# Kernel tuning notes

Measured on AMD Instinct MI355X. Metric: run time of the kernel, lower is better.

The kernel has to match this reference:

```python
import jax, jax.numpy as jnp
import numpy as np

L = 2          # stacked LSTM layers
E = 4          # ensemble size
B, T, D = 256, 256, 512
H, CTX, HID, OUT = 512, 256, 256, 64


def setup_inputs() -> dict:
    key = jax.random.key(0)
    ks = jax.random.split(key, 16)
    w = lambda k, s, sc: (jax.random.normal(k, s, jnp.float32) * sc)
    r1 = lambda k, s: 1.0 + 0.05 * jax.random.normal(k, s, jnp.float32)
    lstm_b = jnp.zeros((L, E, 4 * H), jnp.float32).at[:, :, H:2 * H].set(1.0)  # unit forget bias
    return {
        'sequence_embeddings': jax.random.normal(ks[0], (B, T, D), jnp.float32),
        'context_embeddings': jax.random.normal(ks[1], (B, CTX), jnp.float32),
        'sequence_length': jax.random.randint(ks[2], (B,), 1, T + 1, jnp.int32),
        'lstm_W': w(ks[3], (L, D, 4 * H), 0.02),
        'lstm_U': w(ks[4], (L, H, 4 * H), 0.02),
        'lstm_b': lstm_b,
        'lstm_alpha': r1(ks[5], (L, E, D)),
        'lstm_gamma': r1(ks[6], (L, E, 4 * H)),
        'lstm_ralpha': r1(ks[7], (L, E, H)),
        'lstm_rgamma': r1(ks[8], (L, E, 4 * H)),
        'hid_W': w(ks[9], (H + CTX, HID), 0.05),
        'hid_b': jnp.zeros((E, HID), jnp.float32),
        'hid_alpha': r1(ks[10], (E, H + CTX)),
        'hid_gamma': r1(ks[11], (E, HID)),
        'out_W': w(ks[12], (HID, OUT), 0.05),
        'out_b': jnp.zeros((E, OUT), jnp.float32),
        'out_alpha': r1(ks[13], (E, HID)),
        'out_gamma': r1(ks[14], (E, OUT)),
    }


def reference(sequence_embeddings, context_embeddings, sequence_length,
              lstm_W, lstm_U, lstm_b, lstm_alpha, lstm_gamma, lstm_ralpha, lstm_rgamma,
              hid_W, hid_b, hid_alpha, hid_gamma,
              out_W, out_b, out_alpha, out_gamma):
    Bv, Tv, _ = sequence_embeddings.shape
    Hv = lstm_U.shape[1]
    per = Bv // E  # examples per ensemble member (consecutive blocks)
    exp = lambda p: jnp.repeat(p, per, axis=1)        # [L,E,d] -> [L,B,d]
    aF, gF = exp(lstm_alpha), exp(lstm_gamma)
    raF, rgF = exp(lstm_ralpha), exp(lstm_rgamma)
    bF = exp(lstm_b)

    dt = sequence_embeddings.dtype
    mask = (jnp.arange(Tv)[None, :] < sequence_length[:, None]).astype(dt)  # [B,T]
    xs = (jnp.swapaxes(sequence_embeddings, 0, 1), mask.T[..., None])       # [T,B,D], [T,B,1]

    def step(carry, xm):
        hs, cs = carry
        x, m = xm
        inp = x
        new_h, new_c = [], []
        for l in range(L):
            h, c = hs[l], cs[l]
            # rank-1 multiplicative perturbations fused with gate matmuls
            z = ((inp * aF[l]) @ lstm_W[l]) * gF[l] \
                + ((h * raF[l]) @ lstm_U[l]) * rgF[l] + bF[l]
            i, f, g, o = jnp.split(z, 4, axis=-1)
            c_n = jax.nn.sigmoid(f) * c + jax.nn.sigmoid(i) * jnp.tanh(g)
            h_n = jax.nn.sigmoid(o) * jnp.tanh(c_n)
            h_n = jnp.where(m > 0, h_n, h)  # masked steps carry state through
            c_n = jnp.where(m > 0, c_n, c)
            new_h.append(h_n)
            new_c.append(c_n)
            inp = h_n
        return (jnp.stack(new_h), jnp.stack(new_c)), None

    init = (jnp.zeros((L, Bv, Hv), dt), jnp.zeros((L, Bv, Hv), dt))
    (hs, _), _ = jax.lax.scan(step, init, xs)
    feat = jnp.concatenate([hs[-1], context_embeddings], axis=-1)

    def dense_r1(x, Wt, bt, al, ga, act=None):
        af = jnp.repeat(al, per, axis=0)
        gf = jnp.repeat(ga, per, axis=0)
        bf = jnp.repeat(bt, per, axis=0)
        y = ((x * af) @ Wt) * gf + bf
        return act(y) if act is not None else y

    relu6 = lambda v: jnp.clip(v, 0.0, 6.0)
    hidden = dense_r1(feat, hid_W, hid_b, hid_alpha, hid_gamma, relu6)
    return dense_r1(hidden, out_W, out_b, out_alpha, out_gamma)
```

## Files before the change

### kernel.cpp

```cpp
#include <hip/hip_runtime.h>
#include <cstdint>
#include <cstddef>


typedef __attribute__((ext_vector_type(8))) short  s16x8;
typedef __attribute__((ext_vector_type(8))) __bf16 bf16x8;
typedef __attribute__((ext_vector_type(4))) float  f32x4;
typedef unsigned long long ull;

__device__ __forceinline__ short f2bfs(float f) {
  union { float f; unsigned u; } v; v.f = f;
  unsigned r = v.u + 0x7FFFu + ((v.u >> 16) & 1u);
  return (short)(r >> 16);
}
__device__ __forceinline__ float bf2f(short s) {
  union { unsigned u; float f; } v; v.u = ((unsigned)(unsigned short)s) << 16;
  return v.f;
}
__device__ __forceinline__ void split2(float v, short& hi, short& lo) {
  hi = f2bfs(v);
  lo = f2bfs(v - bf2f(hi));
}
__device__ __forceinline__ float sigf(float x) { return 1.0f / (1.0f + __expf(-x)); }
__device__ __forceinline__ float tanhf_fast(float x) {
  float xc = fminf(fmaxf(x, -15.f), 15.f);
  float e = __expf(2.f * xc);
  return __fdividef(e - 1.f, e + 1.f);
}

__device__ __forceinline__ void unpack_pk(const uint4 r0, const uint4 r1,
                                          s16x8& hi, s16x8& lo) {
  uint4 hv, lv;
  hv.x = __builtin_amdgcn_perm(r0.y, r0.x, 0x05040100u);
  lv.x = __builtin_amdgcn_perm(r0.y, r0.x, 0x07060302u);
  hv.y = __builtin_amdgcn_perm(r0.w, r0.z, 0x05040100u);
  lv.y = __builtin_amdgcn_perm(r0.w, r0.z, 0x07060302u);
  hv.z = __builtin_amdgcn_perm(r1.y, r1.x, 0x05040100u);
  lv.z = __builtin_amdgcn_perm(r1.y, r1.x, 0x07060302u);
  hv.w = __builtin_amdgcn_perm(r1.w, r1.z, 0x05040100u);
  lv.w = __builtin_amdgcn_perm(r1.w, r1.z, 0x07060302u);
  hi = __builtin_bit_cast(s16x8, hv);
  lo = __builtin_bit_cast(s16x8, lv);
}

#define HIP_RLX __ATOMIC_RELAXED
#define HIP_AGT __HIP_MEMORY_SCOPE_AGENT

__device__ __forceinline__ void step_sync(unsigned* grpBase, unsigned* Pme,
                                          unsigned* Pother, int cb,
                                          unsigned tstep, int pneed) {
  __syncthreads();
  if (threadIdx.x < 64) {
    const int lane = threadIdx.x;
    int rel = 0;
    if (lane == 0) {
      unsigned a = __hip_atomic_fetch_add(grpBase + ((cb >> 3) << 4), 1u,
                                          HIP_RLX, HIP_AGT);
      if (a == 8u * tstep - 1u) {
        unsigned r = __hip_atomic_fetch_add(grpBase + 64, 1u, HIP_RLX, HIP_AGT);
        if (r == 4u * tstep - 1u) rel = 1;
      }
    }
    rel = __shfl(rel, 0);
    unsigned* flags = grpBase + 128;
    if (rel) {
      if (lane < 32)
        __hip_atomic_store(flags + lane * 16, tstep, HIP_RLX, HIP_AGT);
      if (lane == 0)
        __hip_atomic_store(Pme, tstep, HIP_RLX, HIP_AGT);
    }
    if (lane == 0) {
      if (!rel) {
        int spins = 0;
        while (__hip_atomic_load(flags + cb * 16, HIP_RLX, HIP_AGT) < tstep) {
          __builtin_amdgcn_s_sleep(1);
          if (++spins > (1 << 24)) break;
        }
      }
      if (pneed > 0) {
        int spins = 0;
        while ((int)__hip_atomic_load(Pother, HIP_RLX, HIP_AGT) < pneed) {
          __builtin_amdgcn_s_sleep(1);
          if (++spins > (1 << 24)) break;
        }
      }
      __builtin_amdgcn_fence(__ATOMIC_ACQUIRE, "agent");
    }
  }
  __syncthreads();
}

#define REDOFF 131072
#define BHU 131072

__global__ __launch_bounds__(512, 1) void lstm_persist(
    const unsigned* __restrict__ seqP,
    unsigned* __restrict__ h0P, unsigned* __restrict__ h1P,
    const short* __restrict__ Wf, const float* __restrict__ biasF,
    const int* __restrict__ slen, unsigned* __restrict__ bar)
{
  extern __shared__ __align__(16) char bsw[];
  const int wg = blockIdx.x;
  const int cls = wg & 7;
  const int layer = cls >> 2;
  const int rb = cls & 3;
  const int cb = wg >> 3;
  const int tid = threadIdx.x;
  const int wave = tid >> 6, lane = tid & 63;
  const int kh = wave >> 2, ws = wave & 3;

  const short* Wfe = Wf + ((size_t)(layer * 4 + rb) * 2048 + cb * 64) * 1024;
  #pragma unroll
  for (int i = 0; i < 16; ++i) {
    int f = (i << 9) + tid;
    int col = f >> 7, fr = f & 127;
    s16x8 v = *reinterpret_cast<const s16x8*>(Wfe + (size_t)col * 1024 + (fr << 3));
    int byo = (fr << 10) + (((col << 4)) ^ ((fr & 7) << 4));
    *reinterpret_cast<s16x8*>(bsw + byo) = v;
  }
  __syncthreads();

  const int j = lane & 15;
  const int g = lane >> 4;
  const int koff = g << 3;
  const int rowg = rb * 64 + ws * 16 + j;
  const int rbase = rb * 64 + ws * 16 + (g << 2);
  const int u = cb * 16 + j;
  const float* bp = biasF + (size_t)(layer * 4 + rb) * 2048 + cb * 64 + j;
  const float bi = bp[0], bff = bp[16], bg = bp[32], bo = bp[48];
  int msl[4];
  #pragma unroll
  for (int r = 0; r < 4; ++r) msl[r] = slen[rbase + r];

  float creg[4] = {0.f, 0.f, 0.f, 0.f};
  float hreg[4] = {0.f, 0.f, 0.f, 0.f};
  unsigned* grpBase = bar + (cls << 10);
  unsigned* Pme     = bar + 8192 + (cls << 4);
  unsigned* Pother  = bar + 8192 + ((cls ^ 4) << 4);
  const int fragbase = kh << 6;

  if (tid == 0) {
    if (layer == 1) {
      int spins = 0;
      while (__hip_atomic_load(Pother, HIP_RLX, HIP_AGT) < 1u) {
        __builtin_amdgcn_s_sleep(1);
        if (++spins > (1 << 24)) break;
      }
    }
    __builtin_amdgcn_fence(__ATOMIC_ACQUIRE, "agent");
  }
  __syncthreads();

  for (int t = 0; t < 256; ++t) {
    const unsigned* ap;
    if (kh == 0) {
      ap = (layer == 0)
         ? seqP + (size_t)t * 131072 + (size_t)rowg * 512 + koff
         : h0P + (size_t)((t + 1) & 3) * BHU + (size_t)rowg * 512 + koff;
    } else {
      ap = (layer == 0)
         ? h0P + (size_t)(t & 3) * BHU + (size_t)rowg * 512 + koff
         : h1P + (size_t)(t & 1) * BHU + (size_t)rowg * 512 + koff;
    }

    uint4 R0[16], R1[16];
    #pragma unroll
    for (int q = 0; q < 16; ++q) {
      R0[q] = *reinterpret_cast<const uint4*>(ap + (q << 5));
      R1[q] = *reinterpret_cast<const uint4*>(ap + (q << 5) + 4);
    }

    f32x4 acc[4] = {}, accL[4] = {};
    #pragma unroll
    for (int q = 0; q < 16; ++q) {
      s16x8 ahi, alo;
      unpack_pk(R0[q], R1[q], ahi, alo);
      const int frag = fragbase + ((q << 2) | g);
      const int fb_ = frag << 10;
      const int xm_ = (frag & 7) << 4;
      #pragma unroll
      for (int cf = 0; cf < 4; ++cf) {
        const int byo_ = fb_ + ((((cf << 8) | (j << 4))) ^ xm_);
        s16x8 b_ = *reinterpret_cast<const s16x8*>(bsw + byo_);
        acc[cf] = __builtin_amdgcn_mfma_f32_16x16x32_bf16(
            __builtin_bit_cast(bf16x8, ahi), __builtin_bit_cast(bf16x8, b_),
            acc[cf], 0, 0, 0);
        accL[cf] = __builtin_amdgcn_mfma_f32_16x16x32_bf16(
            __builtin_bit_cast(bf16x8, alo), __builtin_bit_cast(bf16x8, b_),
            accL[cf], 0, 0, 0);
      }
    }

    if (kh == 1) {
      #pragma unroll
      for (int r = 0; r < 4; ++r) {
        const int lrow = ws * 16 + (g << 2) + r;
        f32x4 v = {acc[0][r] + accL[0][r], acc[1][r] + accL[1][r],
                   acc[2][r] + accL[2][r], acc[3][r] + accL[3][r]};
        *reinterpret_cast<f32x4*>(bsw + REDOFF + lrow * 256 + j * 16) = v;
      }
    }
    __syncthreads();
    if (kh == 0) {
      unsigned* hOut = (layer == 0)
          ? h0P + (size_t)((t + 1) & 3) * BHU
          : h1P + (size_t)((t & 1) ^ 1) * BHU;
      #pragma unroll
      for (int r = 0; r < 4; ++r) {
        const int lrow = ws * 16 + (g << 2) + r;
        f32x4 red = *reinterpret_cast<const f32x4*>(bsw + REDOFF + lrow * 256 + j * 16);
        const int row = rbase + r;
        float zi = acc[0][r] + accL[0][r] + red[0] + bi;
        float zf = acc[1][r] + accL[1][r] + red[1] + bff;
        float zg = acc[2][r] + accL[2][r] + red[2] + bg;
        float zo = acc[3][r] + accL[3][r] + red[3] + bo;
        float cn = sigf(zf) * creg[r] + sigf(zi) * tanhf_fast(zg);
        float hn = sigf(zo) * tanhf_fast(cn);
        if (t >= msl[r]) { cn = creg[r]; hn = hreg[r]; }
        creg[r] = cn; hreg[r] = hn;
        short hh, hl; split2(hn, hh, hl);
        unsigned pk = ((unsigned)(unsigned short)hl << 16)
                    | (unsigned)(unsigned short)hh;
        __hip_atomic_store(&hOut[(size_t)row * 512 + u], pk, HIP_RLX, HIP_AGT);
      }
    }

    int pneed = (t < 255) ? (layer == 0 ? t - 2 : t + 2) : 0;
    step_sync(grpBase, Pme, Pother, cb, (unsigned)(t + 1), pneed);
  }
}

template<int EPI>
__global__ __launch_bounds__(256) void head_gemm(
    const unsigned* __restrict__ a0, int sA0,
    const unsigned* __restrict__ a1, int sA1, int kSplit,
    const short* __restrict__ Wh, const float* __restrict__ bias,
    int N, int K,
    unsigned* __restrict__ outP, float* __restrict__ outf)
{
  const int cb = blockIdx.x, rb = blockIdx.y;
  const int tid = threadIdx.x, wave = tid >> 6, lane = tid & 63;
  const int j = lane & 15;
  const int rowg = rb * 64 + wave * 16 + j;
  const int koff = (lane >> 4) << 3;
  const short* We = Wh + ((size_t)rb * N + cb * 64) * K;
  f32x4 acc[4] = {}, accL[4] = {};
  for (int ks = 0; ks < (K >> 5); ++ks) {
    const int kl = (ks << 5) + koff;
    const unsigned* ap = (kl < kSplit)
        ? (a0 + (size_t)rowg * sA0 + kl)
        : (a1 + (size_t)rowg * sA1 + (kl - kSplit));
    uint4 q0 = *reinterpret_cast<const uint4*>(ap);
    uint4 q1 = *reinterpret_cast<const uint4*>(ap + 4);
    s16x8 ahi, alo; unpack_pk(q0, q1, ahi, alo);
    #pragma unroll
    for (int cf = 0; cf < 4; ++cf) {
      const int ccol = (cf << 4) + j;
      s16x8 b = *reinterpret_cast<const s16x8*>(We + (size_t)ccol * K + kl);
      acc[cf] = __builtin_amdgcn_mfma_f32_16x16x32_bf16(
          __builtin_bit_cast(bf16x8, ahi), __builtin_bit_cast(bf16x8, b),
          acc[cf], 0, 0, 0);
      accL[cf] = __builtin_amdgcn_mfma_f32_16x16x32_bf16(
          __builtin_bit_cast(bf16x8, alo), __builtin_bit_cast(bf16x8, b),
          accL[cf], 0, 0, 0);
    }
  }
  const int rbase = rb * 64 + wave * 16 + ((lane >> 4) << 2);
  #pragma unroll
  for (int cf = 0; cf < 4; ++cf) {
    const int col = cb * 64 + cf * 16 + j;
    const float bb = bias[(size_t)rb * N + col];
    #pragma unroll
    for (int r = 0; r < 4; ++r) {
      float z = acc[cf][r] + accL[cf][r] + bb;
      if (EPI == 1) {
        z = fminf(fmaxf(z, 0.f), 6.f);
        short hh, hl; split2(z, hh, hl);
        outP[(size_t)(rbase + r) * N + col] =
            ((unsigned)(unsigned short)hl << 16) | (unsigned)(unsigned short)hh;
      } else {
        outf[(size_t)(rbase + r) * N + col] = z;
      }
    }
  }
}

__global__ __launch_bounds__(256) void fold_lstm(
    const float* __restrict__ W, const float* __restrict__ U,
    const float* __restrict__ al, const float* __restrict__ ral,
    const float* __restrict__ ga, const float* __restrict__ rga,
    short* __restrict__ Wf)
{
  __shared__ float T[64][65];
  const int tid = threadIdx.x;
  const int kb = blockIdx.x * 64;
  const int cb = blockIdx.y;
  const int le = blockIdx.z;
  const int l  = le >> 2;
  const int kl = tid >> 2;
  const int g  = tid & 3;
  const int k  = kb + kl;
  const bool isW = k < 512;
  const int kk = isW ? k : k - 512;
  const float* src = (isW ? W : U) + ((size_t)l * 512 + kk) * 2048;
  const float  a   = (isW ? al : ral)[(size_t)le * 512 + kk];
  const float* gam = (isW ? ga : rga) + (size_t)le * 2048;
  const int colBase = g * 512 + cb * 16;
  const float4* s4 = reinterpret_cast<const float4*>(src + colBase);
  const float4* g4 = reinterpret_cast<const float4*>(gam + colBase);
  #pragma unroll
  for (int q = 0; q < 4; ++q) {
    float4 v = s4[q], gv = g4[q];
    T[kl][g * 16 + q * 4 + 0] = v.x * a * gv.x;
    T[kl][g * 16 + q * 4 + 1] = v.y * a * gv.y;
    T[kl][g * 16 + q * 4 + 2] = v.z * a * gv.z;
    T[kl][g * 16 + q * 4 + 3] = v.w * a * gv.w;
  }
  __syncthreads();
  const int cl = tid >> 2, kq0 = (tid & 3) * 16;
  alignas(16) short tH[16];
  #pragma unroll
  for (int q = 0; q < 16; ++q) tH[q] = f2bfs(T[kq0 + q][cl]);
  size_t dst = ((size_t)le * 2048 + cb * 64 + cl) * 1024 + kb + kq0;
  *reinterpret_cast<s16x8*>(Wf + dst)     = *reinterpret_cast<s16x8*>(tH);
  *reinterpret_cast<s16x8*>(Wf + dst + 8) = *reinterpret_cast<s16x8*>(tH + 8);
}

__global__ __launch_bounds__(256) void fold_plain(
    const float* __restrict__ src, const float* __restrict__ al,
    const float* __restrict__ ga, short* __restrict__ dst, int N, int K)
{
  __shared__ float T[64][65];
  const int tid = threadIdx.x;
  const int kb = blockIdx.x * 64;
  const int nb = blockIdx.y;
  const int e  = blockIdx.z;
  const int kl = tid >> 2;
  const int c0 = (tid & 3) * 16;
  const int k  = kb + kl;
  const float a = al[(size_t)e * K + k];
  const int colBase = nb * 64 + c0;
  const float4* s4 = reinterpret_cast<const float4*>(src + (size_t)k * N + colBase);
  const float4* g4 = reinterpret_cast<const float4*>(ga + (size_t)e * N + colBase);
  #pragma unroll
  for (int q = 0; q < 4; ++q) {
    float4 v = s4[q], gv = g4[q];
    T[kl][c0 + q * 4 + 0] = v.x * a * gv.x;
    T[kl][c0 + q * 4 + 1] = v.y * a * gv.y;
    T[kl][c0 + q * 4 + 2] = v.z * a * gv.z;
    T[kl][c0 + q * 4 + 3] = v.w * a * gv.w;
  }
  __syncthreads();
  const int cl = tid >> 2, kq0 = (tid & 3) * 16;
  alignas(16) short tH[16];
  #pragma unroll
  for (int q = 0; q < 16; ++q) tH[q] = f2bfs(T[kq0 + q][cl]);
  size_t d = ((size_t)e * N + nb * 64 + cl) * K + kb + kq0;
  *reinterpret_cast<s16x8*>(dst + d)     = *reinterpret_cast<s16x8*>(tH);
  *reinterpret_cast<s16x8*>(dst + d + 8) = *reinterpret_cast<s16x8*>(tH + 8);
}

__global__ void fold_bias_lstm(const float* __restrict__ b, float* __restrict__ bf) {
  int idx = blockIdx.x * 256 + threadIdx.x;
  int cp = idx & 2047, le = idx >> 11;
  int ublk = cp >> 6, g = (cp >> 4) & 3, jj = cp & 15;
  bf[idx] = b[(size_t)le * 2048 + g * 512 + ublk * 16 + jj];
}

__global__ void cvt_pack(const float* __restrict__ s,
                         unsigned* __restrict__ d, int n) {
  int i = blockIdx.x * blockDim.x + threadIdx.x;
  if (i < n) {
    short h, l; split2(s[i], h, l);
    d[i] = ((unsigned)(unsigned short)l << 16) | (unsigned)(unsigned short)h;
  }
}

__global__ __launch_bounds__(128) void pack_seq(const float* __restrict__ s,
                                                unsigned* __restrict__ d) {
  const int t = blockIdx.x;
  const int row = blockIdx.y;
  const int d0 = threadIdx.x * 4;
  float4 v = *reinterpret_cast<const float4*>(
      s + ((size_t)row * 256 + t) * 512 + d0);
  uint4 o; short h, l;
  split2(v.x, h, l); o.x = ((unsigned)(unsigned short)l << 16) | (unsigned)(unsigned short)h;
  split2(v.y, h, l); o.y = ((unsigned)(unsigned short)l << 16) | (unsigned)(unsigned short)h;
  split2(v.z, h, l); o.z = ((unsigned)(unsigned short)l << 16) | (unsigned)(unsigned short)h;
  split2(v.w, h, l); o.w = ((unsigned)(unsigned short)l << 16) | (unsigned)(unsigned short)h;
  *reinterpret_cast<uint4*>(d + ((size_t)t * 256 + row) * 512 + d0) = o;
}

__global__ void zero_ws(float4* p, int n) {
  int i = blockIdx.x * blockDim.x + threadIdx.x;
  if (i < n) p[i] = make_float4(0.f, 0.f, 0.f, 0.f);
}

__global__ void init_bar(unsigned* bar) {
  int i = blockIdx.x * 256 + threadIdx.x;
  if (i < 16384) bar[i] = 0u;
}

constexpr size_t OFF_WF    = 0;
constexpr size_t OFF_WHID  = 33554432;
constexpr size_t OFF_WOUT  = OFF_WHID + 1572864;
constexpr size_t OFF_BIASF = OFF_WOUT + 131072;
constexpr size_t OFF_CTXP  = OFF_BIASF + 65536;
constexpr size_t OFF_H0P   = OFF_CTXP + 262144;
constexpr size_t OFF_H1P   = OFF_H0P + 2097152;
constexpr size_t OFF_HIDP  = OFF_H1P + 1048576;
constexpr size_t OFF_BAR   = OFF_HIDP + 262144;
constexpr size_t OFF_SEQP  = OFF_BAR + 65536;

extern "C" void kernel_launch(void* const* d_in, const int* in_sizes, int n_in,
                              void* d_out, int out_size, void* d_ws, size_t ws_size,
                              hipStream_t stream) {
  (void)in_sizes; (void)n_in; (void)out_size; (void)ws_size;
  const float* seq  = (const float*)d_in[0];
  const float* ctx  = (const float*)d_in[1];
  const int*   slen = (const int*)d_in[2];
  const float* lW   = (const float*)d_in[3];
  const float* lU   = (const float*)d_in[4];
  const float* lb   = (const float*)d_in[5];
  const float* lal  = (const float*)d_in[6];
  const float* lga  = (const float*)d_in[7];
  const float* lral = (const float*)d_in[8];
  const float* lrga = (const float*)d_in[9];
  const float* hW   = (const float*)d_in[10];
  const float* hb   = (const float*)d_in[11];
  const float* hal  = (const float*)d_in[12];
  const float* hga  = (const float*)d_in[13];
  const float* oW   = (const float*)d_in[14];
  const float* ob   = (const float*)d_in[15];
  const float* oal  = (const float*)d_in[16];
  const float* oga  = (const float*)d_in[17];

  char* ws = (char*)d_ws;
  short*    Wf    = (short*)(ws + OFF_WF);
  short*    Whid  = (short*)(ws + OFF_WHID);
  short*    Wout  = (short*)(ws + OFF_WOUT);
  float*    biasF = (float*)(ws + OFF_BIASF);
  unsigned* ctxP  = (unsigned*)(ws + OFF_CTXP);
  unsigned* h0P   = (unsigned*)(ws + OFF_H0P);
  unsigned* h1P   = (unsigned*)(ws + OFF_H1P);
  unsigned* hidP  = (unsigned*)(ws + OFF_HIDP);
  unsigned* bar   = (unsigned*)(ws + OFF_BAR);
  unsigned* seqP  = (unsigned*)(ws + OFF_SEQP);

  (void)hipFuncSetAttribute(reinterpret_cast<const void*>(lstm_persist),
                            hipFuncAttributeMaxDynamicSharedMemorySize, 147456);

  fold_lstm<<<dim3(16, 32, 8), 256, 0, stream>>>(lW, lU, lal, lral, lga, lrga, Wf);
  fold_plain<<<dim3(12, 4, 4), 256, 0, stream>>>(hW, hal, hga, Whid, 256, 768);
  fold_plain<<<dim3(4, 1, 4), 256, 0, stream>>>(oW, oal, oga, Wout, 64, 256);
  fold_bias_lstm<<<64, 256, 0, stream>>>(lb, biasF);
  cvt_pack<<<256, 256, 0, stream>>>(ctx, ctxP, 65536);
  pack_seq<<<dim3(256, 256), 128, 0, stream>>>(seq, seqP);
  zero_ws<<<768, 256, 0, stream>>>((float4*)(ws + OFF_H0P), 3145728 / 16);
  init_bar<<<64, 256, 0, stream>>>(bar);

  lstm_persist<<<256, 512, 147456, stream>>>(seqP, h0P, h1P, Wf, biasF, slen, bar);

  head_gemm<1><<<dim3(4, 4), 256, 0, stream>>>(
      h1P , 512,
      ctxP, 256, 512,
      Whid, hb, 256, 768, hidP, nullptr);
  head_gemm<2><<<dim3(1, 4), 256, 0, stream>>>(
      hidP, 256,
      hidP, 256, 256,
      Wout, ob, 64, 256,
      nullptr, (float*)d_out);
}
```

Before: 3.080 ms.

## Drop bf16 hi/lo split for hidden state and head inputs; flatten step barrier

The recurrent hidden state, context and head activations are now stored as single bf16 values instead of packed hi/lo bf16 pairs. This halves the global traffic of the per-step h exchange and removes half of the MFMAs on the recurrent and head paths. The input-sequence path for layer 0 keeps the split. The two-level atomic arrival counter in the step barrier is also replaced by one counter per group. The trade-offs are lower precision in the recurrent state and more contention on that single atomic.

```diff
diff --git a/kernel.cpp b/kernel.cpp
--- a/kernel.cpp
+++ b/kernel.cpp
@@ -6,7 +6,6 @@
 typedef __attribute__((ext_vector_type(8))) short  s16x8;
 typedef __attribute__((ext_vector_type(8))) __bf16 bf16x8;
 typedef __attribute__((ext_vector_type(4))) float  f32x4;
-typedef unsigned long long ull;
 
 __device__ __forceinline__ short f2bfs(float f) {
   union { float f; unsigned u; } v; v.f = f;
@@ -54,12 +53,8 @@
     const int lane = threadIdx.x;
     int rel = 0;
     if (lane == 0) {
-      unsigned a = __hip_atomic_fetch_add(grpBase + ((cb >> 3) << 4), 1u,
-                                          HIP_RLX, HIP_AGT);
-      if (a == 8u * tstep - 1u) {
-        unsigned r = __hip_atomic_fetch_add(grpBase + 64, 1u, HIP_RLX, HIP_AGT);
-        if (r == 4u * tstep - 1u) rel = 1;
-      }
+      unsigned a = __hip_atomic_fetch_add(grpBase, 1u, HIP_RLX, HIP_AGT);
+      if (a == 32u * tstep - 1u) rel = 1;
     }
     rel = __shfl(rel, 0);
     unsigned* flags = grpBase + 128;
@@ -68,15 +63,14 @@
         __hip_atomic_store(flags + lane * 16, tstep, HIP_RLX, HIP_AGT);
       if (lane == 0)
         __hip_atomic_store(Pme, tstep, HIP_RLX, HIP_AGT);
+    } else if (lane == 0) {
+      int spins = 0;
+      while (__hip_atomic_load(flags + cb * 16, HIP_RLX, HIP_AGT) < tstep) {
+        __builtin_amdgcn_s_sleep(1);
+        if (++spins > (1 << 24)) break;
+      }
     }
     if (lane == 0) {
-      if (!rel) {
-        int spins = 0;
-        while (__hip_atomic_load(flags + cb * 16, HIP_RLX, HIP_AGT) < tstep) {
-          __builtin_amdgcn_s_sleep(1);
-          if (++spins > (1 << 24)) break;
-        }
-      }
       if (pneed > 0) {
         int spins = 0;
         while ((int)__hip_atomic_load(Pother, HIP_RLX, HIP_AGT) < pneed) {
@@ -91,7 +85,7 @@
 }
 
 #define REDOFF 131072
-#define BHU 131072
+#define BHU 65536
 
 __global__ __launch_bounds__(512, 1) void lstm_persist(
     const unsigned* __restrict__ seqP,
@@ -125,7 +119,6 @@
   const int koff = g << 3;
   const int rowg = rb * 64 + ws * 16 + j;
   const int rbase = rb * 64 + ws * 16 + (g << 2);
-  const int u = cb * 16 + j;
   const float* bp = biasF + (size_t)(layer * 4 + rb) * 2048 + cb * 64 + j;
   const float bi = bp[0], bff = bp[16], bg = bp[32], bo = bp[48];
   int msl[4];
@@ -152,42 +145,55 @@
   __syncthreads();
 
   for (int t = 0; t < 256; ++t) {
-    const unsigned* ap;
-    if (kh == 0) {
-      ap = (layer == 0)
-         ? seqP + (size_t)t * 131072 + (size_t)rowg * 512 + koff
-         : h0P + (size_t)((t + 1) & 3) * BHU + (size_t)rowg * 512 + koff;
+    f32x4 acc[4] = {}, accL[4] = {};
+
+    if (kh == 0 && layer == 0) {
+      const unsigned* ap = seqP + (size_t)t * 131072 + (size_t)rowg * 512 + koff;
+      #pragma unroll
+      for (int q = 0; q < 16; ++q) {
+        uint4 r0 = *reinterpret_cast<const uint4*>(ap + (q << 5));
+        uint4 r1 = *reinterpret_cast<const uint4*>(ap + (q << 5) + 4);
+        s16x8 ahi, alo;
+        unpack_pk(r0, r1, ahi, alo);
+        const int frag = (q << 2) | g;
+        const int fb_ = frag << 10;
+        const int xm_ = (frag & 7) << 4;
+        #pragma unroll
+        for (int cf = 0; cf < 4; ++cf) {
+          const int byo_ = fb_ + ((((cf << 8) | (j << 4))) ^ xm_);
+          s16x8 b_ = *reinterpret_cast<const s16x8*>(bsw + byo_);
+          acc[cf] = __builtin_amdgcn_mfma_f32_16x16x32_bf16(
+              __builtin_bit_cast(bf16x8, ahi), __builtin_bit_cast(bf16x8, b_),
+              acc[cf], 0, 0, 0);
+          accL[cf] = __builtin_amdgcn_mfma_f32_16x16x32_bf16(
+              __builtin_bit_cast(bf16x8, alo), __builtin_bit_cast(bf16x8, b_),
+              accL[cf], 0, 0, 0);
+        }
+      }
     } else {
-      ap = (layer == 0)
-         ? h0P + (size_t)(t & 3) * BHU + (size_t)rowg * 512 + koff
-         : h1P + (size_t)(t & 1) * BHU + (size_t)rowg * 512 + koff;
-    }
-
-    uint4 R0[16], R1[16];
-    #pragma unroll
-    for (int q = 0; q < 16; ++q) {
-      R0[q] = *reinterpret_cast<const uint4*>(ap + (q << 5));
-      R1[q] = *reinterpret_cast<const uint4*>(ap + (q << 5) + 4);
-    }
-
-    f32x4 acc[4] = {}, accL[4] = {};
-    #pragma unroll
-    for (int q = 0; q < 16; ++q) {
-      s16x8 ahi, alo;
-      unpack_pk(R0[q], R1[q], ahi, alo);
-      const int frag = fragbase + ((q << 2) | g);
-      const int fb_ = frag << 10;
-      const int xm_ = (frag & 7) << 4;
+      const unsigned* ap;
+      if (kh == 0) {
+        ap = h0P + (size_t)((t + 1) & 3) * BHU + (size_t)rowg * 256 + (g << 2);
+      } else {
+        ap = (layer == 0 ? h0P + (size_t)(t & 3) * BHU
+                         : h1P + (size_t)(t & 1) * BHU)
+           + (size_t)rowg * 256 + (g << 2);
+      }
       #pragma unroll
-      for (int cf = 0; cf < 4; ++cf) {
-        const int byo_ = fb_ + ((((cf << 8) | (j << 4))) ^ xm_);
-        s16x8 b_ = *reinterpret_cast<const s16x8*>(bsw + byo_);
-        acc[cf] = __builtin_amdgcn_mfma_f32_16x16x32_bf16(
-            __builtin_bit_cast(bf16x8, ahi), __builtin_bit_cast(bf16x8, b_),
-            acc[cf], 0, 0, 0);
-        accL[cf] = __builtin_amdgcn_mfma_f32_16x16x32_bf16(
-            __builtin_bit_cast(bf16x8, alo), __builtin_bit_cast(bf16x8, b_),
-            accL[cf], 0, 0, 0);
+      for (int q = 0; q < 16; ++q) {
+        s16x8 a = __builtin_bit_cast(s16x8,
+            *reinterpret_cast<const uint4*>(ap + (q << 4)));
+        const int frag = fragbase + ((q << 2) | g);
+        const int fb_ = frag << 10;
+        const int xm_ = (frag & 7) << 4;
+        #pragma unroll
+        for (int cf = 0; cf < 4; ++cf) {
+          const int byo_ = fb_ + ((((cf << 8) | (j << 4))) ^ xm_);
+          s16x8 b_ = *reinterpret_cast<const s16x8*>(bsw + byo_);
+          acc[cf] = __builtin_amdgcn_mfma_f32_16x16x32_bf16(
+              __builtin_bit_cast(bf16x8, a), __builtin_bit_cast(bf16x8, b_),
+              acc[cf], 0, 0, 0);
+        }
       }
     }
 
@@ -195,8 +201,7 @@
       #pragma unroll
       for (int r = 0; r < 4; ++r) {
         const int lrow = ws * 16 + (g << 2) + r;
-        f32x4 v = {acc[0][r] + accL[0][r], acc[1][r] + accL[1][r],
-                   acc[2][r] + accL[2][r], acc[3][r] + accL[3][r]};
+        f32x4 v = {acc[0][r], acc[1][r], acc[2][r], acc[3][r]};
         *reinterpret_cast<f32x4*>(bsw + REDOFF + lrow * 256 + j * 16) = v;
       }
     }
@@ -218,10 +223,13 @@
         float hn = sigf(zo) * tanhf_fast(cn);
         if (t >= msl[r]) { cn = creg[r]; hn = hreg[r]; }
         creg[r] = cn; hreg[r] = hn;
-        short hh, hl; split2(hn, hh, hl);
-        unsigned pk = ((unsigned)(unsigned short)hl << 16)
-                    | (unsigned)(unsigned short)hh;
-        __hip_atomic_store(&hOut[(size_t)row * 512 + u], pk, HIP_RLX, HIP_AGT);
+        unsigned hu = (unsigned)(unsigned short)f2bfs(hn);
+        unsigned pr = __shfl_xor(hu, 1);
+        if (!(lane & 1)) {
+          __hip_atomic_store(
+              &hOut[(size_t)row * 256 + (cb << 3) + (j >> 1)],
+              (pr << 16) | hu, HIP_RLX, HIP_AGT);
+        }
       }
     }
 
@@ -232,11 +240,11 @@
 
 template<int EPI>
 __global__ __launch_bounds__(256) void head_gemm(
-    const unsigned* __restrict__ a0, int sA0,
-    const unsigned* __restrict__ a1, int sA1, int kSplit,
+    const unsigned short* __restrict__ a0, int sA0,
+    const unsigned short* __restrict__ a1, int sA1, int kSplit,
     const short* __restrict__ Wh, const float* __restrict__ bias,
     int N, int K,
-    unsigned* __restrict__ outP, float* __restrict__ outf)
+    unsigned short* __restrict__ outH, float* __restrict__ outf)
 {
   const int cb = blockIdx.x, rb = blockIdx.y;
   const int tid = threadIdx.x, wave = tid >> 6, lane = tid & 63;
@@ -244,25 +252,20 @@
   const int rowg = rb * 64 + wave * 16 + j;
   const int koff = (lane >> 4) << 3;
   const short* We = Wh + ((size_t)rb * N + cb * 64) * K;
-  f32x4 acc[4] = {}, accL[4] = {};
+  f32x4 acc[4] = {};
   for (int ks = 0; ks < (K >> 5); ++ks) {
     const int kl = (ks << 5) + koff;
-    const unsigned* ap = (kl < kSplit)
+    const unsigned short* ap = (kl < kSplit)
         ? (a0 + (size_t)rowg * sA0 + kl)
         : (a1 + (size_t)rowg * sA1 + (kl - kSplit));
-    uint4 q0 = *reinterpret_cast<const uint4*>(ap);
-    uint4 q1 = *reinterpret_cast<const uint4*>(ap + 4);
-    s16x8 ahi, alo; unpack_pk(q0, q1, ahi, alo);
+    s16x8 a = *reinterpret_cast<const s16x8*>(ap);
     #pragma unroll
     for (int cf = 0; cf < 4; ++cf) {
       const int ccol = (cf << 4) + j;
       s16x8 b = *reinterpret_cast<const s16x8*>(We + (size_t)ccol * K + kl);
       acc[cf] = __builtin_amdgcn_mfma_f32_16x16x32_bf16(
-          __builtin_bit_cast(bf16x8, ahi), __builtin_bit_cast(bf16x8, b),
+          __builtin_bit_cast(bf16x8, a), __builtin_bit_cast(bf16x8, b),
           acc[cf], 0, 0, 0);
-      accL[cf] = __builtin_amdgcn_mfma_f32_16x16x32_bf16(
-          __builtin_bit_cast(bf16x8, alo), __builtin_bit_cast(bf16x8, b),
-          accL[cf], 0, 0, 0);
     }
   }
   const int rbase = rb * 64 + wave * 16 + ((lane >> 4) << 2);
@@ -272,12 +275,10 @@
     const float bb = bias[(size_t)rb * N + col];
     #pragma unroll
     for (int r = 0; r < 4; ++r) {
-      float z = acc[cf][r] + accL[cf][r] + bb;
+      float z = acc[cf][r] + bb;
       if (EPI == 1) {
         z = fminf(fmaxf(z, 0.f), 6.f);
-        short hh, hl; split2(z, hh, hl);
-        outP[(size_t)(rbase + r) * N + col] =
-            ((unsigned)(unsigned short)hl << 16) | (unsigned)(unsigned short)hh;
+        outH[(size_t)(rbase + r) * N + col] = (unsigned short)f2bfs(z);
       } else {
         outf[(size_t)(rbase + r) * N + col] = z;
       }
@@ -367,13 +368,10 @@
   bf[idx] = b[(size_t)le * 2048 + g * 512 + ublk * 16 + jj];
 }
 
-__global__ void cvt_pack(const float* __restrict__ s,
-                         unsigned* __restrict__ d, int n) {
+__global__ void cvt_hi(const float* __restrict__ s,
+                       unsigned short* __restrict__ d, int n) {
   int i = blockIdx.x * blockDim.x + threadIdx.x;
-  if (i < n) {
-    short h, l; split2(s[i], h, l);
-    d[i] = ((unsigned)(unsigned short)l << 16) | (unsigned)(unsigned short)h;
-  }
+  if (i < n) d[i] = (unsigned short)f2bfs(s[i]);
 }
 
 __global__ __launch_bounds__(128) void pack_seq(const float* __restrict__ s,
@@ -405,11 +403,11 @@
 constexpr size_t OFF_WHID  = 33554432;
 constexpr size_t OFF_WOUT  = OFF_WHID + 1572864;
 constexpr size_t OFF_BIASF = OFF_WOUT + 131072;
-constexpr size_t OFF_CTXP  = OFF_BIASF + 65536;
-constexpr size_t OFF_H0P   = OFF_CTXP + 262144;
-constexpr size_t OFF_H1P   = OFF_H0P + 2097152;
-constexpr size_t OFF_HIDP  = OFF_H1P + 1048576;
-constexpr size_t OFF_BAR   = OFF_HIDP + 262144;
+constexpr size_t OFF_CTXH  = OFF_BIASF + 65536;
+constexpr size_t OFF_H0P   = OFF_CTXH + 131072;
+constexpr size_t OFF_H1P   = OFF_H0P + 1048576;
+constexpr size_t OFF_HIDH  = OFF_H1P + 524288;
+constexpr size_t OFF_BAR   = OFF_HIDH + 131072;
 constexpr size_t OFF_SEQP  = OFF_BAR + 65536;
 
 extern "C" void kernel_launch(void* const* d_in, const int* in_sizes, int n_in,
@@ -436,16 +434,16 @@
   const float* oga  = (const float*)d_in[17];
 
   char* ws = (char*)d_ws;
-  short*    Wf    = (short*)(ws + OFF_WF);
-  short*    Whid  = (short*)(ws + OFF_WHID);
-  short*    Wout  = (short*)(ws + OFF_WOUT);
-  float*    biasF = (float*)(ws + OFF_BIASF);
-  unsigned* ctxP  = (unsigned*)(ws + OFF_CTXP);
-  unsigned* h0P   = (unsigned*)(ws + OFF_H0P);
-  unsigned* h1P   = (unsigned*)(ws + OFF_H1P);
-  unsigned* hidP  = (unsigned*)(ws + OFF_HIDP);
-  unsigned* bar   = (unsigned*)(ws + OFF_BAR);
-  unsigned* seqP  = (unsigned*)(ws + OFF_SEQP);
+  short*          Wf    = (short*)(ws + OFF_WF);
+  short*          Whid  = (short*)(ws + OFF_WHID);
+  short*          Wout  = (short*)(ws + OFF_WOUT);
+  float*          biasF = (float*)(ws + OFF_BIASF);
+  unsigned short* ctxH  = (unsigned short*)(ws + OFF_CTXH);
+  unsigned*       h0P   = (unsigned*)(ws + OFF_H0P);
+  unsigned*       h1P   = (unsigned*)(ws + OFF_H1P);
+  unsigned short* hidH  = (unsigned short*)(ws + OFF_HIDH);
+  unsigned*       bar   = (unsigned*)(ws + OFF_BAR);
+  unsigned*       seqP  = (unsigned*)(ws + OFF_SEQP);
 
   (void)hipFuncSetAttribute(reinterpret_cast<const void*>(lstm_persist),
                             hipFuncAttributeMaxDynamicSharedMemorySize, 147456);
@@ -454,20 +452,20 @@
   fold_plain<<<dim3(12, 4, 4), 256, 0, stream>>>(hW, hal, hga, Whid, 256, 768);
   fold_plain<<<dim3(4, 1, 4), 256, 0, stream>>>(oW, oal, oga, Wout, 64, 256);
   fold_bias_lstm<<<64, 256, 0, stream>>>(lb, biasF);
-  cvt_pack<<<256, 256, 0, stream>>>(ctx, ctxP, 65536);
+  cvt_hi<<<256, 256, 0, stream>>>(ctx, ctxH, 65536);
   pack_seq<<<dim3(256, 256), 128, 0, stream>>>(seq, seqP);
-  zero_ws<<<768, 256, 0, stream>>>((float4*)(ws + OFF_H0P), 3145728 / 16);
+  zero_ws<<<384, 256, 0, stream>>>((float4*)(ws + OFF_H0P), 1572864 / 16);
   init_bar<<<64, 256, 0, stream>>>(bar);
 
   lstm_persist<<<256, 512, 147456, stream>>>(seqP, h0P, h1P, Wf, biasF, slen, bar);
 
   head_gemm<1><<<dim3(4, 4), 256, 0, stream>>>(
-      h1P , 512,
-      ctxP, 256, 512,
-      Whid, hb, 256, 768, hidP, nullptr);
+      (const unsigned short*)h1P , 512,
+      ctxH, 256, 512,
+      Whid, hb, 256, 768, hidH, nullptr);
   head_gemm<2><<<dim3(1, 4), 256, 0, stream>>>(
-      hidP, 256,
-      hidP, 256, 256,
+      hidH, 256,
+      hidH, 256, 256,
       Wout, ob, 64, 256,
       nullptr, (float*)d_out);
 }
```

Result: faster. 2.759 ms, median of 2 (-10.4%).
